# Performance work log

Hardware: AMD Instinct MI355X
Metric: run time of the kernel (lower is better)

## Reference

```python
import jax, jax.numpy as jnp
import numpy as np

BITWIDTH = 8
Q_FRAC = BITWIDTH - 4                       # fractional bits of output quantizer
Q_SCALE = 2.0 ** Q_FRAC                     # 16
QMAX = (2 ** (BITWIDTH - 1) - 1) / Q_SCALE  # 7.9375 (overflow clamp on accumulator)
QMIN = -8.0                                 # underflow clamp / accumulator init
LUT_IN_SCALE = 4096.0                       # diff quantized to Q12 index
LUT_IN_MAX = 32767.0                        # index clamp
LUT_OUT_SCALE = 65536.0                     # look_up (= table/2) lives on a 1/65536 grid


def _lut(diff):
    # Emulates the hex lookup table: table[i]/2 ~= log(1 + exp(-i/4096)),
    # quantized to the 1/65536 grid (table entries are Q15, then halved).
    d_int = jnp.minimum(jnp.floor(diff * LUT_IN_SCALE), LUT_IN_MAX)
    d_q = d_int / LUT_IN_SCALE
    return jnp.round(jnp.log1p(jnp.exp(-d_q)) * LUT_OUT_SCALE) / LUT_OUT_SCALE


def _quant_feature(x):
    # QuantizeFeature(bitwidth, bitwidth-4): round to 1/16 grid, clamp to int8 range.
    q = jnp.clip(jnp.round(x * Q_SCALE), -(2 ** (BITWIDTH - 1)), 2 ** (BITWIDTH - 1) - 1)
    return q / Q_SCALE


def _quantized_log_softmax(x):
    B, C, H, W = x.shape
    flat = x.reshape(B * C, H, W)  # sequential axis = flattened batch*channel (as in source)
    init = jnp.full((H, W), QMIN, dtype=x.dtype)

    def step(sum_exp, t):  # t: [H, W]
        diff = jnp.abs(sum_exp - t)
        lu = _lut(diff)
        # if sum_exp > t: sum_exp += lu else: sum_exp = t + lu  ==  max(sum_exp, t) + lu
        s = jnp.maximum(sum_exp, t) + lu
        s = jnp.clip(s, QMIN, QMAX)  # overflow/underflow clamps
        return s, None

    sum_exp, _ = jax.lax.scan(step, init, flat)
    # final scalar per spatial location is broadcast to every (b, c)
    return _quant_feature(x - sum_exp[None, None, :, :])


def setup_inputs() -> dict:
    key = jax.random.key(0)
    x = jax.random.normal(key, (4, 64, 384, 384), dtype=jnp.float32)
    return {"x": x}


def reference(x):
    return _quantized_log_softmax(x)
```

## Files before the change

kernel.cpp:

```cpp
#include <hip/hip_runtime.h>
#include <math.h>

#define QLS_T   256
#define QLS_HW  (384 * 384)
#define CHUNK   8
#define TPC     (QLS_T / CHUNK)

#define Q_SCALE      16.0f
#define INV_Q_SCALE  (1.0f / 16.0f)
#define QMAXF        7.9375f
#define QMINF        (-8.0f)
#define LUT_IN_SCALE 4096.0f
#define LUT_IN_MAX   32767.0f
#define INV_LUT_OUT  (1.0f / 65536.0f)

#define NEG_LOG2E_DIV (-1.4426950408889634f / 4096.0f)
#define LN2_X_65536   45426.09375f

__device__ __forceinline__ float qls_step(float s, float v) {
    float diff = fabsf(s - v);
    float d_int = fminf(floorf(diff * LUT_IN_SCALE), LUT_IN_MAX);
    float e  = __builtin_amdgcn_exp2f(d_int * NEG_LOG2E_DIV);
    float lu = rintf(__builtin_amdgcn_logf(1.0f + e) * LN2_X_65536) * INV_LUT_OUT;
    s = fmaxf(s, v) + lu;
    return fminf(fmaxf(s, QMINF), QMAXF);
}

__global__ __launch_bounds__(512, 4) void qls_chunked_kernel(
    const float* __restrict__ x, float* __restrict__ out) {
    const int lane  = threadIdx.x & 63;
    const int chunk = threadIdx.x >> 6;
    const int loc   = blockIdx.x * 64 + lane;
    const size_t base = (size_t)loc + (size_t)chunk * TPC * QLS_HW;
    const float* xp = x + base;

    float v[TPC];
    #pragma unroll
    for (int k = 0; k < TPC; ++k) v[k] = xp[(size_t)k * QLS_HW];

    float s = QMINF;
    #pragma unroll
    for (int k = 0; k < TPC; ++k) s = qls_step(s, v[k]);

    __shared__ float part[CHUNK][64];
    part[chunk][lane] = s;
    __syncthreads();

    float tot = part[0][lane];
    #pragma unroll
    for (int c = 1; c < CHUNK; ++c) tot = qls_step(tot, part[c][lane]);

    float* op = out + base;
    #pragma unroll
    for (int k = 0; k < TPC; ++k) {
        float q = fminf(fmaxf(rintf((v[k] - tot) * Q_SCALE), -128.0f), 127.0f);
        __builtin_nontemporal_store(q * INV_Q_SCALE, op + (size_t)k * QLS_HW);
    }
}

extern "C" void kernel_launch(void* const* d_in, const int* in_sizes, int n_in,
                              void* d_out, int out_size, void* d_ws, size_t ws_size,
                              hipStream_t stream) {
    const float* x = (const float*)d_in[0];
    float* out = (float*)d_out;
    const int blocks = QLS_HW / 64;
    qls_chunked_kernel<<<blocks, 512, 0, stream>>>(x, out);
}
```

Before: 268.0 us.

## Process four locations per thread with float4 loads and 16 chunks

Each thread now handles four adjacent spatial locations using vectorized float4 loads and stores, running four independent scan chains to expose instruction-level parallelism. The channel axis is split into 16 chunks (one per wave) in 1024-thread blocks, which shortens each serial chain. Inputs are no longer held in registers; they are re-read from memory for the output pass, which adds read traffic but lowers register pressure.

```diff
diff --git a/kernel.cpp b/kernel.cpp
--- a/kernel.cpp
+++ b/kernel.cpp
@@ -3,8 +3,9 @@
 
 #define QLS_T   256
 #define QLS_HW  (384 * 384)
-#define CHUNK   8
+#define CHUNK   16
 #define TPC     (QLS_T / CHUNK)
+#define LPB     256
 
 #define Q_SCALE      16.0f
 #define INV_Q_SCALE  (1.0f / 16.0f)
@@ -17,6 +18,8 @@
 #define NEG_LOG2E_DIV (-1.4426950408889634f / 4096.0f)
 #define LN2_X_65536   45426.09375f
 
+typedef float f32x4 __attribute__((ext_vector_type(4)));
+
 __device__ __forceinline__ float qls_step(float s, float v) {
     float diff = fabsf(s - v);
     float d_int = fminf(floorf(diff * LUT_IN_SCALE), LUT_IN_MAX);
@@ -26,35 +29,46 @@
     return fminf(fmaxf(s, QMINF), QMAXF);
 }
 
-__global__ __launch_bounds__(512, 4) void qls_chunked_kernel(
+__global__ __launch_bounds__(1024, 4) void qls_f4_kernel(
     const float* __restrict__ x, float* __restrict__ out) {
-    const int lane  = threadIdx.x & 63;
-    const int chunk = threadIdx.x >> 6;
-    const int loc   = blockIdx.x * 64 + lane;
-    const size_t base = (size_t)loc + (size_t)chunk * TPC * QLS_HW;
+    const int lane = threadIdx.x & 63;
+    const int w    = threadIdx.x >> 6;
+    const int loc  = blockIdx.x * LPB + lane * 4;
+    const size_t base = (size_t)w * TPC * QLS_HW + loc;
     const float* xp = x + base;
 
-    float v[TPC];
+    float s0 = QMINF, s1 = QMINF, s2 = QMINF, s3 = QMINF;
     #pragma unroll
-    for (int k = 0; k < TPC; ++k) v[k] = xp[(size_t)k * QLS_HW];
+    for (int k = 0; k < TPC; ++k) {
+        f32x4 v = *reinterpret_cast<const f32x4*>(xp + (size_t)k * QLS_HW);
+        s0 = qls_step(s0, v.x); s1 = qls_step(s1, v.y);
+        s2 = qls_step(s2, v.z); s3 = qls_step(s3, v.w);
+    }
 
-    float s = QMINF;
-    #pragma unroll
-    for (int k = 0; k < TPC; ++k) s = qls_step(s, v[k]);
-
-    __shared__ float part[CHUNK][64];
-    part[chunk][lane] = s;
+    __shared__ float part[CHUNK][LPB];
+    f32x4 sv; sv.x = s0; sv.y = s1; sv.z = s2; sv.w = s3;
+    *reinterpret_cast<f32x4*>(&part[w][lane * 4]) = sv;
     __syncthreads();
 
-    float tot = part[0][lane];
+    f32x4 t4 = *reinterpret_cast<const f32x4*>(&part[0][lane * 4]);
+    float t0 = t4.x, t1 = t4.y, t2 = t4.z, t3 = t4.w;
     #pragma unroll
-    for (int c = 1; c < CHUNK; ++c) tot = qls_step(tot, part[c][lane]);
+    for (int c = 1; c < CHUNK; ++c) {
+        f32x4 p4 = *reinterpret_cast<const f32x4*>(&part[c][lane * 4]);
+        t0 = qls_step(t0, p4.x); t1 = qls_step(t1, p4.y);
+        t2 = qls_step(t2, p4.z); t3 = qls_step(t3, p4.w);
+    }
 
     float* op = out + base;
     #pragma unroll
     for (int k = 0; k < TPC; ++k) {
-        float q = fminf(fmaxf(rintf((v[k] - tot) * Q_SCALE), -128.0f), 127.0f);
-        __builtin_nontemporal_store(q * INV_Q_SCALE, op + (size_t)k * QLS_HW);
+        f32x4 v = *reinterpret_cast<const f32x4*>(xp + (size_t)k * QLS_HW);
+        f32x4 q;
+        q.x = fminf(fmaxf(rintf((v.x - t0) * Q_SCALE), -128.0f), 127.0f) * INV_Q_SCALE;
+        q.y = fminf(fmaxf(rintf((v.y - t1) * Q_SCALE), -128.0f), 127.0f) * INV_Q_SCALE;
+        q.z = fminf(fmaxf(rintf((v.z - t2) * Q_SCALE), -128.0f), 127.0f) * INV_Q_SCALE;
+        q.w = fminf(fmaxf(rintf((v.w - t3) * Q_SCALE), -128.0f), 127.0f) * INV_Q_SCALE;
+        __builtin_nontemporal_store(q, reinterpret_cast<f32x4*>(op + (size_t)k * QLS_HW));
     }
 }
 
@@ -63,6 +77,6 @@
                               hipStream_t stream) {
     const float* x = (const float*)d_in[0];
     float* out = (float*)d_out;
-    const int blocks = QLS_HW / 64;
-    qls_chunked_kernel<<<blocks, 512, 0, stream>>>(x, out);
+    const int blocks = QLS_HW / LPB;
+    qls_f4_kernel<<<blocks, 1024, 0, stream>>>(x, out);
 }
```

After: 277.8 us. 1.04x slower.

## Split scan into three kernels with workspace partials and vectorized loads

Applied to the files above, without the earlier changes.

Replaces the single fused kernel with three passes. The first does per-chunk scans over 16 chunks using float4 loads, the second merges the chunk partials per location into a final sum buffer, and the third re-reads x and writes the quantized output with float4 non-temporal stores. The aim is to remove the register pressure from holding 32 values per thread and to raise occupancy and memory-level parallelism through vector loads. The cost is a second full read of x, extra workspace traffic and two more launches. The old fused kernel is kept as a fallback for when no workspace is available.

```diff
diff --git a/kernel.cpp b/kernel.cpp
--- a/kernel.cpp
+++ b/kernel.cpp
@@ -1,10 +1,13 @@
 #include <hip/hip_runtime.h>
 #include <math.h>
 
-#define QLS_T   256
-#define QLS_HW  (384 * 384)
-#define CHUNK   8
-#define TPC     (QLS_T / CHUNK)
+#define QLS_T    256
+#define QLS_HW   (384 * 384)
+#define QLS_HW4  (QLS_HW / 4)
+#define CHUNK    16
+#define TPC      (QLS_T / CHUNK)
+#define TILES    36
+#define TILE_LOC 4096
 
 #define Q_SCALE      16.0f
 #define INV_Q_SCALE  (1.0f / 16.0f)
@@ -17,6 +20,8 @@
 #define NEG_LOG2E_DIV (-1.4426950408889634f / 4096.0f)
 #define LN2_X_65536   45426.09375f
 
+typedef float f32x4 __attribute__((ext_vector_type(4)));
+
 __device__ __forceinline__ float qls_step(float s, float v) {
     float diff = fabsf(s - v);
     float d_int = fminf(floorf(diff * LUT_IN_SCALE), LUT_IN_MAX);
@@ -26,33 +31,88 @@
     return fminf(fmaxf(s, QMINF), QMAXF);
 }
 
-__global__ __launch_bounds__(512, 4) void qls_chunked_kernel(
+__global__ __launch_bounds__(1024) void qls_k1_scan(
+    const float* __restrict__ x, float* __restrict__ part) {
+    const int c    = blockIdx.x / TILES;
+    const int tile = blockIdx.x % TILES;
+    const int loc  = tile * TILE_LOC + threadIdx.x * 4;
+    const float* xp = x + (size_t)c * TPC * QLS_HW + loc;
+
+    float s0 = QMINF, s1 = QMINF, s2 = QMINF, s3 = QMINF;
+    #pragma unroll
+    for (int k = 0; k < TPC; ++k) {
+        f32x4 v = *reinterpret_cast<const f32x4*>(xp + (size_t)k * QLS_HW);
+        s0 = qls_step(s0, v.x); s1 = qls_step(s1, v.y);
+        s2 = qls_step(s2, v.z); s3 = qls_step(s3, v.w);
+    }
+    f32x4 sv; sv.x = s0; sv.y = s1; sv.z = s2; sv.w = s3;
+    *reinterpret_cast<f32x4*>(part + (size_t)c * QLS_HW + loc) = sv;
+}
+
+__global__ __launch_bounds__(256) void qls_k2_merge(
+    const float* __restrict__ part, float* __restrict__ sbuf) {
+    const int loc = (blockIdx.x * 256 + threadIdx.x) * 4;
+    f32x4 t4 = *reinterpret_cast<const f32x4*>(part + loc);
+    float t0 = t4.x, t1 = t4.y, t2 = t4.z, t3 = t4.w;
+    #pragma unroll
+    for (int c = 1; c < CHUNK; ++c) {
+        f32x4 p4 = *reinterpret_cast<const f32x4*>(part + (size_t)c * QLS_HW + loc);
+        t0 = qls_step(t0, p4.x); t1 = qls_step(t1, p4.y);
+        t2 = qls_step(t2, p4.z); t3 = qls_step(t3, p4.w);
+    }
+    f32x4 sv; sv.x = t0; sv.y = t1; sv.z = t2; sv.w = t3;
+    *reinterpret_cast<f32x4*>(sbuf + loc) = sv;
+}
+
+__global__ __launch_bounds__(256) void qls_k3_out(
+    const float* __restrict__ x, const float* __restrict__ sbuf,
+    float* __restrict__ out) {
+    const int idx  = blockIdx.x * 256 + threadIdx.x;
+    const int loc4 = idx % QLS_HW4;
+    const int tb   = (idx / QLS_HW4) * 4;
+
+    const f32x4 s4 = reinterpret_cast<const f32x4*>(sbuf)[loc4];
+
+    #pragma unroll
+    for (int k = 0; k < 4; ++k) {
+        const int t = tb + k;
+        const f32x4 v = reinterpret_cast<const f32x4*>(x + (size_t)t * QLS_HW)[loc4];
+        f32x4 q;
+        q.x = fminf(fmaxf(rintf((v.x - s4.x) * Q_SCALE), -128.0f), 127.0f) * INV_Q_SCALE;
+        q.y = fminf(fmaxf(rintf((v.y - s4.y) * Q_SCALE), -128.0f), 127.0f) * INV_Q_SCALE;
+        q.z = fminf(fmaxf(rintf((v.z - s4.z) * Q_SCALE), -128.0f), 127.0f) * INV_Q_SCALE;
+        q.w = fminf(fmaxf(rintf((v.w - s4.w) * Q_SCALE), -128.0f), 127.0f) * INV_Q_SCALE;
+        __builtin_nontemporal_store(q, reinterpret_cast<f32x4*>(out + (size_t)t * QLS_HW) + loc4);
+    }
+}
+
+__global__ __launch_bounds__(512, 4) void qls_fused_kernel(
     const float* __restrict__ x, float* __restrict__ out) {
     const int lane  = threadIdx.x & 63;
     const int chunk = threadIdx.x >> 6;
     const int loc   = blockIdx.x * 64 + lane;
-    const size_t base = (size_t)loc + (size_t)chunk * TPC * QLS_HW;
+    const size_t base = (size_t)loc + (size_t)chunk * 32 * QLS_HW;
     const float* xp = x + base;
 
-    float v[TPC];
+    float v[32];
     #pragma unroll
-    for (int k = 0; k < TPC; ++k) v[k] = xp[(size_t)k * QLS_HW];
+    for (int k = 0; k < 32; ++k) v[k] = xp[(size_t)k * QLS_HW];
 
     float s = QMINF;
     #pragma unroll
-    for (int k = 0; k < TPC; ++k) s = qls_step(s, v[k]);
+    for (int k = 0; k < 32; ++k) s = qls_step(s, v[k]);
 
-    __shared__ float part[CHUNK][64];
+    __shared__ float part[8][64];
     part[chunk][lane] = s;
     __syncthreads();
 
     float tot = part[0][lane];
     #pragma unroll
-    for (int c = 1; c < CHUNK; ++c) tot = qls_step(tot, part[c][lane]);
+    for (int c = 1; c < 8; ++c) tot = qls_step(tot, part[c][lane]);
 
     float* op = out + base;
     #pragma unroll
-    for (int k = 0; k < TPC; ++k) {
+    for (int k = 0; k < 32; ++k) {
         float q = fminf(fmaxf(rintf((v[k] - tot) * Q_SCALE), -128.0f), 127.0f);
         __builtin_nontemporal_store(q * INV_Q_SCALE, op + (size_t)k * QLS_HW);
     }
@@ -63,6 +123,16 @@
                               hipStream_t stream) {
     const float* x = (const float*)d_in[0];
     float* out = (float*)d_out;
-    const int blocks = QLS_HW / 64;
-    qls_chunked_kernel<<<blocks, 512, 0, stream>>>(x, out);
+    const size_t part_bytes = (size_t)CHUNK * QLS_HW * sizeof(float);
+    const size_t s_bytes    = (size_t)QLS_HW * sizeof(float);
+
+    if (d_ws != nullptr && ws_size >= part_bytes + s_bytes) {
+        float* part = (float*)d_ws;
+        float* sbuf = part + (size_t)CHUNK * QLS_HW;
+        qls_k1_scan <<<CHUNK * TILES, 1024, 0, stream>>>(x, part);
+        qls_k2_merge<<<QLS_HW4 / 256, 256, 0, stream>>>(part, sbuf);
+        qls_k3_out  <<<(QLS_T / 4) * (QLS_HW4 / 256), 256, 0, stream>>>(x, sbuf, out);
+    } else {
+        qls_fused_kernel<<<QLS_HW / 64, 512, 0, stream>>>(x, out);
+    }
 }
```

Result: slower. 279.8 us (+4.4%).
